# Kernel optimization log

Hardware: AMD Instinct MI355X
Metric: run time of the kernel (lower is better)

Reference implementation:

```python
import jax, jax.numpy as jnp
import numpy as np

E = 64          # num_expert
DIN = 512       # d_input
DOUT = 512      # d_output
T = 131072      # total routed tokens (sum of fwd_expert_count)


def setup_inputs() -> dict:
    key = jax.random.key(0)
    k1, k2, k3 = jax.random.split(key, 3)
    inp = jax.random.normal(k1, (T, DIN), dtype=jnp.float32)
    # FMoELinear params: weight [E, d_out, d_in], bias [E, d_out]
    weight = jax.random.normal(k2, (E, DOUT, DIN), dtype=jnp.float32) * (1.0 / np.sqrt(DIN))
    bias = jax.random.normal(k3, (E, DOUT), dtype=jnp.float32) * 0.01
    # Irregular per-expert token counts summing exactly to T (host-side int64,
    # as in fastmoe where fwd_expert_count lives on CPU and drives dispatch).
    rng = np.random.default_rng(0)
    counts = rng.multinomial(T, np.full(E, 1.0 / E))
    fwd_expert_count = np.asarray(counts, dtype=np.int64)
    return {"inp": inp, "weight": weight, "bias": bias, "fwd_expert_count": fwd_expert_count}


def reference(inp, weight, bias, fwd_expert_count):
    # Grouped GEMM: tokens are sorted by expert; expert e owns rows
    # [offs[e], offs[e+1]).  y_i = x_i @ W_e^T + b_e.
    counts = np.asarray(fwd_expert_count)
    offs = np.concatenate([[0], np.cumsum(counts)])
    outs = []
    for e in range(counts.shape[0]):  # fixed small loop over experts
        xe = inp[int(offs[e]):int(offs[e + 1])]          # [n_e, d_in]
        outs.append(xe @ weight[e].T + bias[e])          # [n_e, d_out]
    return jnp.concatenate(outs, axis=0)                 # [T, d_out]
```

## Files before the change

### kernel.cpp

```cpp
#include <hip/hip_runtime.h>
#include <hip/hip_bf16.h>
#include <stdint.h>

#define NE    64
#define DIN   512
#define DOUT  512
#define TTOK  131072
#define BM    256
#define BN    256
#define BK    64
#define NKT   (DIN / BK)
#define TILES_TOTAL (TTOK / BM + NE)
#define NXCD  8
#define TPX   (TILES_TOTAL / NXCD)

typedef __bf16 bf16x8_t __attribute__((ext_vector_type(8)));
typedef float  f32x4_t  __attribute__((ext_vector_type(4)));

#define ABUF(i) ((i) * 32768)
#define BBUF(i) (65536 + (i) * 32768)
#define LDS_BYTES 131072

#define WAITV(n) asm volatile("s_waitcnt vmcnt(" #n ")" ::: "memory")
#define LGKM0()  asm volatile("s_waitcnt lgkmcnt(0)" ::: "memory")
#define SB() __builtin_amdgcn_sched_barrier(0)
#define BAR() __builtin_amdgcn_s_barrier()

#define WBF_OFF 32768

__global__ void setup_tiles(const int* __restrict__ cnt, int* __restrict__ ws) {
    int e = threadIdx.x;
    if (e >= NE) return;
    int off = 0, tbase = 0;
    for (int i = 0; i < e; ++i) {
        int c = cnt[i];
        off += c;
        tbase += (c + (BM - 1)) / BM;
    }
    int c = cnt[e];
    int nt = (c + (BM - 1)) / BM;
    int* tbl = ws + 4;
    for (int t = 0; t < nt; ++t) {
        int idx = tbase + t;
        tbl[4 * idx + 0] = e;
        tbl[4 * idx + 1] = off + t * BM;
        tbl[4 * idx + 2] = off + c;
        tbl[4 * idx + 3] = 0;
    }
    if (e == NE - 1) ws[0] = tbase + nt;
}

__global__ __launch_bounds__(256) void wcvt(const float* __restrict__ w,
                                            __bf16* __restrict__ wbf) {
    const size_t stride = (size_t)gridDim.x * 256;
    size_t i = (size_t)blockIdx.x * 256 + threadIdx.x;
    const size_t n8 = (size_t)NE * DOUT * DIN / 8;
    for (; i < n8; i += stride) {
        f32x4_t a = *(const f32x4_t*)(w + i * 8);
        f32x4_t b = *(const f32x4_t*)(w + i * 8 + 4);
        bf16x8_t h;
#pragma unroll
        for (int j = 0; j < 4; ++j) {
            h[j]     = (__bf16)a[j];
            h[4 + j] = (__bf16)b[j];
        }
        *(bf16x8_t*)(wbf + i * 8) = h;
    }
}

__device__ __forceinline__ void gload16(const void* g, uint8_t* l) {
    __builtin_amdgcn_global_load_lds(
        (const __attribute__((address_space(1))) uint32_t*)g,
        (__attribute__((address_space(3))) uint32_t*)l, 16, 0, 0);
}

__global__ __launch_bounds__(512, 2) void moe_gemm(
    const float* __restrict__ inp,
    const __bf16* __restrict__ wbf,
    const float* __restrict__ bias,
    const int* __restrict__ ws,
    float* __restrict__ out)
{
    __shared__ __align__(16) uint8_t smem[LDS_BYTES];

    const int bid  = blockIdx.x;
    const int xcd  = bid & (NXCD - 1);
    const int slot = bid >> 3;
    const int tile = xcd * TPX + (slot >> 1);
    const int n0   = (slot & 1) * BN;

    const int ntiles = ws[0];
    if (tile >= ntiles) return;
    const int4 ti = ((const int4*)(ws + 4))[tile];
    const int e = ti.x, row0 = ti.y, row_end = ti.z;

    const int tid  = threadIdx.x;
    const int lane = tid & 63;
    const int wave = tid >> 6;

    const int arow = tid >> 3;
    const int acn  = tid & 7;
    const int aswz = (arow & 7) << 4;
    const float* asrc[4];
    int awoff[4];
#pragma unroll
    for (int i = 0; i < 4; ++i) {
        int r = arow + 64 * i;
        int grow = row0 + r;
        if (grow > row_end - 1) grow = row_end - 1;
        asrc[i]  = inp + (size_t)grow * DIN + acn * 8;
        awoff[i] = r * 128 + ((acn * 16) ^ aswz);
    }
    f32x4_t ra[8];
    auto issueAglb = [&](int tk) {
#pragma unroll
        for (int i = 0; i < 4; ++i) {
            ra[2 * i]     = *(const f32x4_t*)(asrc[i] + tk * BK);
            ra[2 * i + 1] = *(const f32x4_t*)(asrc[i] + tk * BK + 4);
        }
    };
    auto cvtWriteA = [&](int buf) {
#pragma unroll
        for (int i = 0; i < 4; ++i) {
            bf16x8_t h;
#pragma unroll
            for (int j = 0; j < 4; ++j) {
                h[j]     = (__bf16)ra[2 * i][j];
                h[4 + j] = (__bf16)ra[2 * i + 1][j];
            }
            *(bf16x8_t*)(smem + ABUF(buf) + awoff[i]) = h;
        }
    };

    const int dr = lane >> 3;
    const int ac = lane & 7;
    const int u  = ac ^ dr;
    const __bf16* bsrc[4];
#pragma unroll
    for (int i = 0; i < 4; ++i) {
        int row = wave * 32 + i * 8 + dr;
        bsrc[i] = wbf + (size_t)(e * DOUT + n0 + row) * DIN + u * 8;
    }
    auto issueB = [&](int tk, int buf) {
        uint8_t* dst = smem + BBUF(buf) + wave * 4096;
#pragma unroll
        for (int i = 0; i < 4; ++i)
            gload16(bsrc[i] + tk * BK, dst + i * 1024);
    };

    const int wr = (wave >> 2) * 128;
    const int wc = (wave & 3) * 64;
    const int frow = lane & 15;
    const int kg   = lane >> 4;

    f32x4_t acc[8][4] = {};
    bf16x8_t bg[4][2], af[2][2];

    auto dsrB = [&](int buf) {
#pragma unroll
        for (int n = 0; n < 4; ++n) {
            const int row = wc + n * 16 + frow;
            const uint8_t* p = smem + BBUF(buf) + row * 128;
            const int sw = (row & 7) << 4;
#pragma unroll
            for (int ks = 0; ks < 2; ++ks)
                bg[n][ks] = *(const bf16x8_t*)(p + ((ks * 64 + kg * 16) ^ sw));
        }
    };
    auto dsrA = [&](int buf, int q) {
#pragma unroll
        for (int j = 0; j < 2; ++j) {
            const int row = wr + (2 * q + j) * 16 + frow;
            const uint8_t* p = smem + ABUF(buf) + row * 128;
            const int sw = (row & 7) << 4;
#pragma unroll
            for (int ks = 0; ks < 2; ++ks)
                af[j][ks] = *(const bf16x8_t*)(p + ((ks * 64 + kg * 16) ^ sw));
        }
    };
    auto mfmaQ = [&](int q) {
        __builtin_amdgcn_s_setprio(1);
#pragma unroll
        for (int ks = 0; ks < 2; ++ks)
#pragma unroll
            for (int j = 0; j < 2; ++j)
#pragma unroll
                for (int n = 0; n < 4; ++n)
                    acc[2 * q + j][n] = __builtin_amdgcn_mfma_f32_16x16x32_bf16(
                        af[j][ks], bg[n][ks], acc[2 * q + j][n], 0, 0, 0);
        __builtin_amdgcn_s_setprio(0);
    };

    issueAglb(0);
    issueB(0, 0);
    WAITV(4); SB();
    cvtWriteA(0);
    issueAglb(1);
    WAITV(8); LGKM0(); SB();
    BAR();

#pragma unroll
    for (int t = 0; t < NKT; ++t) {
        const int buf = t & 1;
        if (t + 1 < NKT) {
            WAITV(0); SB();
            cvtWriteA(buf ^ 1);
            issueB(t + 1, buf ^ 1); SB();
        }
        dsrB(buf);
        dsrA(buf, 0); SB();
        BAR(); LGKM0(); SB();
        mfmaQ(0);
        BAR();
        if (t + 2 < NKT) { issueAglb(t + 2); SB(); }
        dsrA(buf, 1); SB();
        BAR(); LGKM0(); SB();
        mfmaQ(1);
        BAR();
        dsrA(buf, 2); SB();
        BAR(); LGKM0(); SB();
        mfmaQ(2);
        BAR();
        dsrA(buf, 3);
        if (t + 1 < NKT) {
            if (t + 2 < NKT) { WAITV(8); } else { WAITV(0); }
        }
        SB();
        BAR(); LGKM0(); SB();
        mfmaQ(3);
        BAR();
    }

    const int crow = kg * 4;
    const int ccol = frow;
    float bv[4];
#pragma unroll
    for (int n = 0; n < 4; ++n)
        bv[n] = bias[e * DOUT + n0 + wc + n * 16 + ccol];
#pragma unroll
    for (int m = 0; m < 8; ++m) {
#pragma unroll
        for (int j = 0; j < 4; ++j) {
            const int grow = row0 + wr + m * 16 + crow + j;
            if (grow < row_end) {
                float* orow = out + (size_t)grow * DOUT + n0 + wc + ccol;
#pragma unroll
                for (int n = 0; n < 4; ++n)
                    orow[n * 16] = acc[m][n][j] + bv[n];
            }
        }
    }
}

extern "C" void kernel_launch(void* const* d_in, const int* in_sizes, int n_in,
                              void* d_out, int out_size, void* d_ws, size_t ws_size,
                              hipStream_t stream) {
    const float* inp    = (const float*)d_in[0];
    const float* weight = (const float*)d_in[1];
    const float* bias   = (const float*)d_in[2];
    const int* cnt      = (const int*)d_in[3];
    float* out = (float*)d_out;
    int* ws = (int*)d_ws;
    __bf16* wbf = (__bf16*)((char*)d_ws + WBF_OFF);

    hipLaunchKernelGGL(setup_tiles, dim3(1), dim3(64), 0, stream, cnt, ws);
    hipLaunchKernelGGL(wcvt, dim3(2048), dim3(256), 0, stream, weight, wbf);
    hipLaunchKernelGGL(moe_gemm, dim3(TILES_TOTAL * 2), dim3(512), 0, stream,
                       inp, wbf, bias, ws, out);
}
```

Baseline: 192.8 us.

## Halve M tile, single-buffer A in LDS, target four blocks per CU

Shrinks the M tile from 256 to 128 rows, cutting LDS use (A tile single-buffered) and per-thread accumulators so four 512-thread blocks can fit per CU instead of two. The A-tile pipeline is restructured: the next A slice is loaded only one step ahead into registers and written to LDS after the last fragment read, while B stays double-buffered. The aim is more occupancy and less padding waste on the irregular per-expert tiles. In exchange, arithmetic intensity per block drops, B traffic per output doubles, and there is less prefetch depth for A.

```diff
diff --git a/kernel.cpp b/kernel.cpp
--- a/kernel.cpp
+++ b/kernel.cpp
@@ -6,7 +6,7 @@
 #define DIN   512
 #define DOUT  512
 #define TTOK  131072
-#define BM    256
+#define BM    128
 #define BN    256
 #define BK    64
 #define NKT   (DIN / BK)
@@ -17,9 +17,9 @@
 typedef __bf16 bf16x8_t __attribute__((ext_vector_type(8)));
 typedef float  f32x4_t  __attribute__((ext_vector_type(4)));
 
-#define ABUF(i) ((i) * 32768)
-#define BBUF(i) (65536 + (i) * 32768)
-#define LDS_BYTES 131072
+#define ABUF    0
+#define BBUF(i) (16384 + (i) * 32768)
+#define LDS_BYTES 81920
 
 #define WAITV(n) asm volatile("s_waitcnt vmcnt(" #n ")" ::: "memory")
 #define LGKM0()  asm volatile("s_waitcnt lgkmcnt(0)" ::: "memory")
@@ -74,7 +74,7 @@
         (__attribute__((address_space(3))) uint32_t*)l, 16, 0, 0);
 }
 
-__global__ __launch_bounds__(512, 2) void moe_gemm(
+__global__ __launch_bounds__(512, 4) void moe_gemm(
     const float* __restrict__ inp,
     const __bf16* __restrict__ wbf,
     const float* __restrict__ bias,
@@ -98,38 +98,34 @@
     const int lane = tid & 63;
     const int wave = tid >> 6;
 
-    const int arow = tid >> 3;
-    const int acn  = tid & 7;
+    const int arow = tid >> 2;
+    const int acn  = tid & 3;
+    int agrow = row0 + arow;
+    if (agrow > row_end - 1) agrow = row_end - 1;
+    const float* asrc = inp + (size_t)agrow * DIN + acn * 8;
     const int aswz = (arow & 7) << 4;
-    const float* asrc[4];
-    int awoff[4];
-#pragma unroll
-    for (int i = 0; i < 4; ++i) {
-        int r = arow + 64 * i;
-        int grow = row0 + r;
-        if (grow > row_end - 1) grow = row_end - 1;
-        asrc[i]  = inp + (size_t)grow * DIN + acn * 8;
-        awoff[i] = r * 128 + ((acn * 16) ^ aswz);
-    }
-    f32x4_t ra[8];
+    const int awoff0 = arow * 128 + ((acn * 16) ^ aswz);
+    const int awoff1 = arow * 128 + (((acn + 4) * 16) ^ aswz);
+
+    f32x4_t ra[4];
     auto issueAglb = [&](int tk) {
-#pragma unroll
-        for (int i = 0; i < 4; ++i) {
-            ra[2 * i]     = *(const f32x4_t*)(asrc[i] + tk * BK);
-            ra[2 * i + 1] = *(const f32x4_t*)(asrc[i] + tk * BK + 4);
-        }
-    };
-    auto cvtWriteA = [&](int buf) {
-#pragma unroll
-        for (int i = 0; i < 4; ++i) {
-            bf16x8_t h;
-#pragma unroll
-            for (int j = 0; j < 4; ++j) {
-                h[j]     = (__bf16)ra[2 * i][j];
-                h[4 + j] = (__bf16)ra[2 * i + 1][j];
-            }
-            *(bf16x8_t*)(smem + ABUF(buf) + awoff[i]) = h;
-        }
+        const float* p = asrc + tk * BK;
+        ra[0] = *(const f32x4_t*)(p);
+        ra[1] = *(const f32x4_t*)(p + 4);
+        ra[2] = *(const f32x4_t*)(p + 32);
+        ra[3] = *(const f32x4_t*)(p + 36);
+    };
+    auto cvtWriteA = [&]() {
+        bf16x8_t h0, h1;
+#pragma unroll
+        for (int j = 0; j < 4; ++j) {
+            h0[j]     = (__bf16)ra[0][j];
+            h0[4 + j] = (__bf16)ra[1][j];
+            h1[j]     = (__bf16)ra[2][j];
+            h1[4 + j] = (__bf16)ra[3][j];
+        }
+        *(bf16x8_t*)(smem + ABUF + awoff0) = h0;
+        *(bf16x8_t*)(smem + ABUF + awoff1) = h1;
     };
 
     const int dr = lane >> 3;
@@ -148,13 +144,13 @@
             gload16(bsrc[i] + tk * BK, dst + i * 1024);
     };
 
-    const int wr = (wave >> 2) * 128;
+    const int wr = (wave >> 2) * 64;
     const int wc = (wave & 3) * 64;
     const int frow = lane & 15;
     const int kg   = lane >> 4;
 
-    f32x4_t acc[8][4] = {};
-    bf16x8_t bg[4][2], af[2][2];
+    f32x4_t acc[4][4] = {};
+    bf16x8_t bg[4][2], af[2];
 
     auto dsrB = [&](int buf) {
 #pragma unroll
@@ -167,67 +163,61 @@
                 bg[n][ks] = *(const bf16x8_t*)(p + ((ks * 64 + kg * 16) ^ sw));
         }
     };
-    auto dsrA = [&](int buf, int q) {
-#pragma unroll
-        for (int j = 0; j < 2; ++j) {
-            const int row = wr + (2 * q + j) * 16 + frow;
-            const uint8_t* p = smem + ABUF(buf) + row * 128;
-            const int sw = (row & 7) << 4;
-#pragma unroll
-            for (int ks = 0; ks < 2; ++ks)
-                af[j][ks] = *(const bf16x8_t*)(p + ((ks * 64 + kg * 16) ^ sw));
-        }
+    auto dsrA = [&](int q) {
+        const int row = wr + q * 16 + frow;
+        const uint8_t* p = smem + ABUF + row * 128;
+        const int sw = (row & 7) << 4;
+#pragma unroll
+        for (int ks = 0; ks < 2; ++ks)
+            af[ks] = *(const bf16x8_t*)(p + ((ks * 64 + kg * 16) ^ sw));
     };
     auto mfmaQ = [&](int q) {
         __builtin_amdgcn_s_setprio(1);
 #pragma unroll
         for (int ks = 0; ks < 2; ++ks)
 #pragma unroll
-            for (int j = 0; j < 2; ++j)
-#pragma unroll
-                for (int n = 0; n < 4; ++n)
-                    acc[2 * q + j][n] = __builtin_amdgcn_mfma_f32_16x16x32_bf16(
-                        af[j][ks], bg[n][ks], acc[2 * q + j][n], 0, 0, 0);
+            for (int n = 0; n < 4; ++n)
+                acc[q][n] = __builtin_amdgcn_mfma_f32_16x16x32_bf16(
+                    af[ks], bg[n][ks], acc[q][n], 0, 0, 0);
         __builtin_amdgcn_s_setprio(0);
     };
 
     issueAglb(0);
     issueB(0, 0);
     WAITV(4); SB();
-    cvtWriteA(0);
-    issueAglb(1);
-    WAITV(8); LGKM0(); SB();
+    cvtWriteA();
+    LGKM0();
+    WAITV(0); SB();
     BAR();
 
 #pragma unroll
     for (int t = 0; t < NKT; ++t) {
-        const int buf = t & 1;
+        const int bb = t & 1;
+        if (t + 1 < NKT) { issueB(t + 1, bb ^ 1); SB(); }
+        dsrB(bb);
+        dsrA(0); SB();
+        BAR(); LGKM0(); SB();
+        mfmaQ(0);
+        BAR();
+        if (t + 1 < NKT) { issueAglb(t + 1); SB(); }
+        dsrA(1); SB();
+        BAR(); LGKM0(); SB();
+        mfmaQ(1);
+        BAR();
+        dsrA(2); SB();
+        BAR(); LGKM0(); SB();
+        mfmaQ(2);
+        BAR();
+        dsrA(3);
+        LGKM0(); SB();
+        BAR();
         if (t + 1 < NKT) {
             WAITV(0); SB();
-            cvtWriteA(buf ^ 1);
-            issueB(t + 1, buf ^ 1); SB();
-        }
-        dsrB(buf);
-        dsrA(buf, 0); SB();
-        BAR(); LGKM0(); SB();
-        mfmaQ(0);
-        BAR();
-        if (t + 2 < NKT) { issueAglb(t + 2); SB(); }
-        dsrA(buf, 1); SB();
-        BAR(); LGKM0(); SB();
-        mfmaQ(1);
-        BAR();
-        dsrA(buf, 2); SB();
-        BAR(); LGKM0(); SB();
-        mfmaQ(2);
-        BAR();
-        dsrA(buf, 3);
-        if (t + 1 < NKT) {
-            if (t + 2 < NKT) { WAITV(8); } else { WAITV(0); }
-        }
+            cvtWriteA();
+        }
+        mfmaQ(3);
+        if (t + 1 < NKT) { LGKM0(); }
         SB();
-        BAR(); LGKM0(); SB();
-        mfmaQ(3);
         BAR();
     }
 
@@ -238,7 +228,7 @@
     for (int n = 0; n < 4; ++n)
         bv[n] = bias[e * DOUT + n0 + wc + n * 16 + ccol];
 #pragma unroll
-    for (int m = 0; m < 8; ++m) {
+    for (int m = 0; m < 4; ++m) {
 #pragma unroll
         for (int j = 0; j < 4; ++j) {
             const int grow = row0 + wr + m * 16 + crow + j;
```

New measurement: 303.5 us. 57.4% more time.
